# Kernel optimization log

Measured on AMD Instinct MI355X. Metric: run time of the kernel, lower is better.

Reference implementation:

```python
import jax, jax.numpy as jnp
import numpy as np

B, T, D, H, DEPTH, FF, NC = 512, 150, 256, 8, 6, 1024, 4
HD = D // H  # head dim = 32


def setup_inputs() -> dict:
    key = jax.random.key(0)
    ks = iter(jax.random.split(key, 64))
    n = lambda shape, s=0.02: jax.random.normal(next(ks), shape, jnp.float32) * s
    return dict(
        token_types=jax.random.randint(next(ks), (B, T), 0, 4, jnp.int32),
        decision_ids=jax.random.randint(next(ks), (B, T), 0, NC, jnp.int32),
        action_vals=jax.random.normal(next(ks), (B, T, 1), jnp.float32),
        dis_vals=jax.random.normal(next(ks), (B, T, 10), jnp.float32),
        v_vals=jax.random.normal(next(ks), (B, T, 3), jnp.float32),
        action_W=n((1, D), 0.5), action_b=n((D,)),
        dis_W=n((10, D), 0.2), dis_b=n((D,)),
        v_W=n((3, D), 0.3), v_b=n((D,)),
        decision_table=n((NC, D)),
        pos_embed=n((1, T + 1, D)), cls_token=n((1, 1, D)),
        qkv_W=n((DEPTH, D, 3 * D), 0.05), qkv_b=jnp.zeros((DEPTH, 3 * D), jnp.float32),
        out_W=n((DEPTH, D, D), 0.05), out_b=jnp.zeros((DEPTH, D), jnp.float32),
        ln1_g=jnp.ones((DEPTH, D), jnp.float32), ln1_b=jnp.zeros((DEPTH, D), jnp.float32),
        ln2_g=jnp.ones((DEPTH, D), jnp.float32), ln2_b=jnp.zeros((DEPTH, D), jnp.float32),
        ffn1_W=n((DEPTH, D, FF), 0.05), ffn1_b=jnp.zeros((DEPTH, FF), jnp.float32),
        ffn2_W=n((DEPTH, FF, D), 0.05), ffn2_b=jnp.zeros((DEPTH, D), jnp.float32),
        dec_ln_g=jnp.ones((D,), jnp.float32), dec_ln_b=jnp.zeros((D,), jnp.float32),
        dec_W=n((D, NC), 0.05), dec_b=jnp.zeros((NC,), jnp.float32),
        act_ln_g=jnp.ones((D,), jnp.float32), act_ln_b=jnp.zeros((D,), jnp.float32),
        act_W=n((D, 1), 0.05), act_b=jnpp if False else jnp.zeros((1,), jnp.float32),
    )


def _ln(x, g, b):
    # PyTorch LayerNorm: eps=1e-5, biased variance
    m = jnp.mean(x, axis=-1, keepdims=True)
    v = jnp.mean(jnp.square(x - m), axis=-1, keepdims=True)
    return (x - m) * jax.lax.rsqrt(v + 1e-5) * g + b


def reference(token_types, decision_ids, action_vals, dis_vals, v_vals,
              action_W, action_b, dis_W, dis_b, v_W, v_b, decision_table,
              pos_embed, cls_token, qkv_W, qkv_b, out_W, out_b,
              ln1_g, ln1_b, ln2_g, ln2_b, ffn1_W, ffn1_b, ffn2_W, ffn2_b,
              dec_ln_g, dec_ln_b, dec_W, dec_b, act_ln_g, act_ln_b, act_W, act_b):
    # --- batched type-dispatched token embedding (replaces the per-token python loop) ---
    a_emb = action_vals @ action_W + action_b                     # [B,T,D] type 'A'
    s_emb = dis_vals @ dis_W + dis_b + v_vals @ v_W + v_b         # [B,T,D] type 'S'
    d_emb = decision_table[decision_ids]                          # [B,T,D] type 'D'
    t = token_types[..., None]
    x = jnp.where(t == 0, a_emb, jnp.where(t == 1, s_emb, jnp.where(t == 2, d_emb, 0.0)))
    # --- prepend CLS, add positional embedding ---
    x = jnp.concatenate([jnp.broadcast_to(cls_token, (x.shape[0], 1, D)), x], axis=1)
    S = x.shape[1]
    x = x + pos_embed[:, :S, :]
    # --- post-norm TransformerEncoder (PyTorch default: ReLU FFN, norm_first=False, eval/no dropout) ---
    scale = 1.0 / np.sqrt(HD).astype(np.float32)
    for i in range(DEPTH):
        qkv = x @ qkv_W[i] + qkv_b[i]                             # [B,S,3D]
        q, k, v = jnp.split(qkv, 3, axis=-1)
        q = q.reshape(-1, S, H, HD)
        k = k.reshape(-1, S, H, HD)
        v = v.reshape(-1, S, H, HD)
        att = jax.nn.softmax(jnp.einsum('bqhd,bkhd->bhqk', q, k) * scale, axis=-1)
        o = jnp.einsum('bhqk,bkhd->bqhd', att, v).reshape(-1, S, D)
        x = _ln(x + o @ out_W[i] + out_b[i], ln1_g[i], ln1_b[i])
        ff = jax.nn.relu(x @ ffn1_W[i] + ffn1_b[i]) @ ffn2_W[i] + ffn2_b[i]
        x = _ln(x + ff, ln2_g[i], ln2_b[i])
    cls = x[:, 0, :]
    decision_logits = _ln(cls, dec_ln_g, dec_ln_b) @ dec_W + dec_b   # [B,4]
    action_pred = _ln(cls, act_ln_g, act_ln_b) @ act_W + act_b       # [B,1]
    return (decision_logits, action_pred)
```

## Files before the change

kernel.cpp:

```cpp
#include <hip/hip_runtime.h>
#include <hip/hip_bf16.h>

typedef __hip_bfloat16 bf16;
typedef unsigned short u16;
typedef __attribute__((ext_vector_type(8))) short s16x8;
typedef __attribute__((ext_vector_type(4))) float f32x4;

#define B_ 512
#define T_ 150
#define S_ 151
#define D_ 256
#define H_ 8
#define HD_ 32
#define FF_ 1024
#define NC_ 4
#define DEPTH_ 6
#define MTOT 77312
#define MT128 (MTOT / 128)
#define MT64 (MTOT / 64)

#define XOFF 0
#define C1OFF (MTOT * D_)
#define C2OFF (C1OFF + MTOT * FF_)
#define WSELEMS (C2OFF + MTOT * D_)

#define QKVT_OFF 0
#define OUTT_OFF (QKVT_OFF + DEPTH_ * D_ * 768)
#define FFN1T_OFF (OUTT_OFF + DEPTH_ * D_ * D_)
#define FFN2T_OFF (FFN1T_OFF + DEPTH_ * D_ * FF_)
#define WTELEMS (FFN2T_OFF + DEPTH_ * FF_ * D_)

__device__ __align__(16) u16 g_ws[WSELEMS];
__device__ __align__(16) u16 g_wt[WTELEMS];
__device__ int g_f32flag;

__device__ __forceinline__ float ldf(const void* p, size_t i, int f) {
  return f ? ((const float*)p)[i] : __bfloat162float(((const bf16*)p)[i]);
}
__device__ __forceinline__ float b2f(u16 u) {
  union { unsigned int i; float f; } v; v.i = ((unsigned int)u) << 16; return v.f;
}
__device__ __forceinline__ u16 f2b(float x) {
  bf16 h = __float2bfloat16(x);
  return *reinterpret_cast<u16*>(&h);
}

typedef __attribute__((address_space(3))) void lds_void;
typedef const __attribute__((address_space(1))) void glob_void;
__device__ __forceinline__ void gload_lds16(const u16* g, u16* l) {
  __builtin_amdgcn_global_load_lds((glob_void*)g, (lds_void*)l, 16, 0, 0);
}

#define PROBE_N 38656
__global__ __launch_bounds__(256) void probe_kernel(const void* pe)
{
  const u16* w = (const u16*)pe;
  int susp = 0, zeroEven = 0;
  for (int k = threadIdx.x; k < PROBE_N; k += 256) {
    u16 u = w[k];
    int ex = (u >> 7) & 0xFF;
    if (ex >= 141) susp++;
    if ((k & 1) == 0 && (u & 0x7FFF) == 0) zeroEven++;
  }
  __shared__ int s_susp, s_zero;
  if (threadIdx.x == 0) { s_susp = 0; s_zero = 0; }
  __syncthreads();
  atomicAdd(&s_susp, susp);
  atomicAdd(&s_zero, zeroEven);
  __syncthreads();
  if (threadIdx.x == 0)
    g_f32flag = (s_susp > 0 || s_zero >= ((PROBE_N / 2) * 9) / 10) ? 1 : 0;
}

__global__ __launch_bounds__(256) void wtrans_kernel(const void* src, int dstOff,
                                                     int K, int N, int total)
{
  const int f = g_f32flag;
  int idx = blockIdx.x * 256 + threadIdx.x;
  if (idx >= total) return;
  int kn = K * N;
  int l = idx / kn;
  int r = idx - l * kn;
  int k = r / N;
  int n = r - k * N;
  g_wt[dstOff + (size_t)l * kn + (size_t)n * K + k] = f2b(ldf(src, idx, f));
}

__global__ __launch_bounds__(256) void embed_kernel(
    const int* __restrict__ tt, const int* __restrict__ dids,
    const void* av, const void* dv, const void* vv,
    const void* aW, const void* ab, const void* dW, const void* db,
    const void* vW, const void* vb, const void* table, const void* pos,
    const void* cls)
{
  const int f = g_f32flag;
  u16* x = g_ws + XOFF;
  int row = blockIdx.x;
  int d = threadIdx.x;
  int b = row / S_;
  int s = row - b * S_;
  float val;
  if (s == 0) {
    val = ldf(cls, d, f);
  } else {
    int t = s - 1;
    int idx = b * T_ + t;
    int ty = tt[idx];
    if (ty == 0) {
      val = ldf(av, idx, f) * ldf(aW, d, f) + ldf(ab, d, f);
    } else if (ty == 1) {
      float acc = ldf(db, d, f) + ldf(vb, d, f);
#pragma unroll
      for (int i = 0; i < 10; i++) acc += ldf(dv, (size_t)idx * 10 + i, f) * ldf(dW, i * D_ + d, f);
#pragma unroll
      for (int i = 0; i < 3; i++) acc += ldf(vv, (size_t)idx * 3 + i, f) * ldf(vW, i * D_ + d, f);
      val = acc;
    } else if (ty == 2) {
      int did = dids[idx] & (NC_ - 1);
      val = ldf(table, (size_t)did * D_ + d, f);
    } else {
      val = 0.f;
    }
  }
  val += ldf(pos, s * D_ + d, f);
  x[(size_t)row * D_ + d] = f2b(val);
}

__global__ __launch_bounds__(256, 3) void gemm_mfma(
    int aOff, int wtOff, const void* bias, size_t bOff,
    int cOff, int N, int K, int relu, int NB, int tiledC)
{
  const int f = g_f32flag;
  const u16* A = g_ws + aOff;
  const u16* Bt = g_wt + wtOff;
  u16* C = g_ws + cOff;
  __shared__ __align__(16) u16 sm[16384];
  const int tid = threadIdx.x;

  int gblk = blockIdx.x;
  int bm, bn;
  {
    const int full = (MT128 / 8) * 8;
    if (gblk < NB * full) {
      int per = NB * 8;
      int grp = gblk / per, rem = gblk % per;
      bm = grp * 8 + (rem & 7);
      bn = rem >> 3;
    } else {
      int id = gblk - NB * full;
      bm = full + id / NB;
      bn = id % NB;
    }
  }

  const int lane = tid & 63, wid = tid >> 6;
  const int wm = (wid >> 1) * 64, wn = (wid & 1) * 64;
  const int frow = lane & 15, quad = lane >> 4;

  const int rg = lane >> 3;
  const int ck = ((lane & 7) ^ rg) * 8;
  const u16* Ag[4]; const u16* Bg[4];
  u16 *Asl[4], *Bsl[4];
#pragma unroll
  for (int p = 0; p < 4; p++) {
    int grp = wid * 4 + p;
    int row = grp * 8 + rg;
    Ag[p] = A + (size_t)(bm * 128 + row) * K + ck;
    Bg[p] = Bt + (size_t)(bn * 128 + row) * K + ck;
    Asl[p] = &sm[grp * 512];
    Bsl[p] = &sm[8192 + grp * 512];
  }

  f32x4 acc[4][4] = {};

  for (int kt = 0; kt < K; kt += 64) {
    if (kt) __syncthreads();
#pragma unroll
    for (int p = 0; p < 4; p++) {
      gload_lds16(Ag[p] + kt, Asl[p]);
      gload_lds16(Bg[p] + kt, Bsl[p]);
    }
    __syncthreads();
#pragma unroll
    for (int s = 0; s < 2; s++) {
      s16x8 af[4], bfr[4];
      const int cfr = ((s * 4 + quad) ^ (frow & 7)) * 8;
#pragma unroll
      for (int t = 0; t < 4; t++) {
        af[t]  = *(const s16x8*)&sm[(wm + t * 16 + frow) * 64 + cfr];
        bfr[t] = *(const s16x8*)&sm[8192 + (wn + t * 16 + frow) * 64 + cfr];
      }
#pragma unroll
      for (int mt = 0; mt < 4; mt++)
#pragma unroll
        for (int nt = 0; nt < 4; nt++)
          acc[mt][nt] = __builtin_amdgcn_mfma_f32_16x16x32_bf16(af[mt], bfr[nt], acc[mt][nt], 0, 0, 0);
    }
  }

  float bv[4];
#pragma unroll
  for (int nt = 0; nt < 4; nt++)
    bv[nt] = ldf(bias, bOff + (size_t)(bn * 128 + wn + nt * 16 + frow), f);
  __syncthreads();
#pragma unroll
  for (int p = 0; p < 2; p++) {
    if ((wid >> 1) == p) {
#pragma unroll
      for (int mt = 0; mt < 4; mt++)
#pragma unroll
        for (int nt = 0; nt < 4; nt++)
#pragma unroll
          for (int r = 0; r < 4; r++) {
            int rl = (wm & 63) + mt * 16 + quad * 4 + r;
            float v = acc[mt][nt][r] + bv[nt];
            if (relu) v = fmaxf(v, 0.f);
            sm[rl * 136 + wn + nt * 16 + frow] = f2b(v);
          }
    }
    __syncthreads();
    {
      int rl = tid >> 2;
      int cq = (tid & 3) * 32;
      if (!tiledC) {
        size_t gb = (size_t)(bm * 128 + p * 64 + rl) * N + bn * 128 + cq;
#pragma unroll
        for (int j = 0; j < 4; j++)
          *(s16x8*)(C + gb + j * 8) = *(const s16x8*)&sm[rl * 136 + cq + j * 8];
      } else {
        const size_t tmBase = (size_t)(bm * 2 + p) * (N >> 6);
#pragma unroll
        for (int j = 0; j < 4; j++) {
          int col = bn * 128 + cq + j * 8;
          size_t addr = ((tmBase + (col >> 6)) << 12) + (rl << 6) + (col & 63);
          *(s16x8*)(C + addr) = *(const s16x8*)&sm[rl * 136 + cq + j * 8];
        }
      }
    }
    __syncthreads();
  }
}

#define LNHALF 20480

__global__ __launch_bounds__(256, 2) void gemm_ln(
    int aOff, int wtOff, const void* bias, size_t bOff,
    const void* lng, const void* lnb, size_t lnOff, int K)
{
  const int f = g_f32flag;
  const u16* A = g_ws + aOff;
  const u16* Bt = g_wt + wtOff;
  __shared__ __align__(16) u16 sm[2 * LNHALF];
  const int tid = threadIdx.x;
  const int bm = blockIdx.x;
  const int lane = tid & 63, wid = tid >> 6;
  const int wn = wid * 64;
  const int frow = lane & 15, quad = lane >> 4;
  const int rg = lane >> 3;
  const int ck = ((lane & 7) ^ rg) * 8;

  const u16* Ag[2]; u16* Asl[2];
  const u16* Bg[8]; u16* Bsl[8];
#pragma unroll
  for (int p = 0; p < 2; p++) {
    int grp = wid * 2 + p;
    Ag[p] = A + ((size_t)bm * (K >> 6) << 12) + ((grp * 8 + rg) << 6) + ck;
    Asl[p] = &sm[grp * 512];
  }
#pragma unroll
  for (int p = 0; p < 8; p++) {
    int grp = wid * 8 + p;
    Bg[p] = Bt + (size_t)(grp * 8 + rg) * K + ck;
    Bsl[p] = &sm[4096 + grp * 512];
  }

  f32x4 acc[4][4] = {};
  const int nsteps = K >> 6;

#pragma unroll
  for (int p = 0; p < 2; p++) gload_lds16(Ag[p], Asl[p]);
#pragma unroll
  for (int p = 0; p < 8; p++) gload_lds16(Bg[p], Bsl[p]);
  __syncthreads();

  for (int t = 0; t < nsteps; t++) {
    const int cur = (t & 1) * LNHALF;
    if (t + 1 < nsteps) {
      const int nxt = ((t + 1) & 1) * LNHALF;
      const int ktA = (t + 1) << 12;
      const int ktB = (t + 1) << 6;
#pragma unroll
      for (int p = 0; p < 2; p++) gload_lds16(Ag[p] + ktA, Asl[p] + nxt);
#pragma unroll
      for (int p = 0; p < 8; p++) gload_lds16(Bg[p] + ktB, Bsl[p] + nxt);
    }
#pragma unroll
    for (int s = 0; s < 2; s++) {
      s16x8 af[4], bfr[4];
      const int cfr = ((s * 4 + quad) ^ (frow & 7)) * 8;
#pragma unroll
      for (int ti = 0; ti < 4; ti++) {
        af[ti]  = *(const s16x8*)&sm[cur + (ti * 16 + frow) * 64 + cfr];
        bfr[ti] = *(const s16x8*)&sm[cur + 4096 + (wn + ti * 16 + frow) * 64 + cfr];
      }
#pragma unroll
      for (int mt = 0; mt < 4; mt++)
#pragma unroll
        for (int nt = 0; nt < 4; nt++)
          acc[mt][nt] = __builtin_amdgcn_mfma_f32_16x16x32_bf16(af[mt], bfr[nt], acc[mt][nt], 0, 0, 0);
    }
    __syncthreads();
  }

  const int rl = tid >> 2;
  const int cq = (tid & 3) * 64;
  const size_t rowg = (size_t)bm * 64 + rl;
  s16x8 xr[8];
#pragma unroll
  for (int j = 0; j < 8; j++)
    xr[j] = *(const s16x8*)(g_ws + XOFF + rowg * 256 + cq + j * 8);

  float bv[4];
#pragma unroll
  for (int nt = 0; nt < 4; nt++)
    bv[nt] = ldf(bias, bOff + (size_t)(wn + nt * 16 + frow), f);
#pragma unroll
  for (int mt = 0; mt < 4; mt++)
#pragma unroll
    for (int nt = 0; nt < 4; nt++)
#pragma unroll
      for (int r = 0; r < 4; r++) {
        int row = mt * 16 + quad * 4 + r;
        int col = wn + nt * 16 + frow;
        sm[row * 264 + col] = f2b(acc[mt][nt][r] + bv[nt]);
      }
  __syncthreads();
  {
    float s1 = 0.f, s2 = 0.f;
#pragma unroll
    for (int j = 0; j < 8; j++) {
      s16x8 yv = *(const s16x8*)&sm[rl * 264 + cq + j * 8];
#pragma unroll
      for (int e = 0; e < 8; e++) {
        float v = b2f((u16)yv[e]) + b2f((u16)xr[j][e]);
        s1 += v; s2 += v * v;
      }
    }
    s1 += __shfl_xor(s1, 1, 64); s2 += __shfl_xor(s2, 1, 64);
    s1 += __shfl_xor(s1, 2, 64); s2 += __shfl_xor(s2, 2, 64);
    float mean = s1 * (1.f / 256.f);
    float var = s2 * (1.f / 256.f) - mean * mean;
    float rs = rsqrtf(var + 1e-5f);
#pragma unroll
    for (int j = 0; j < 8; j++) {
      s16x8 yv = *(const s16x8*)&sm[rl * 264 + cq + j * 8];
      s16x8 ov;
#pragma unroll
      for (int e = 0; e < 8; e++) {
        float v = b2f((u16)yv[e]) + b2f((u16)xr[j][e]);
        int col = cq + j * 8 + e;
        ov[e] = (short)f2b((v - mean) * rs * ldf(lng, lnOff + col, f) + ldf(lnb, lnOff + col, f));
      }
      *(s16x8*)(g_ws + XOFF + rowg * 256 + cq + j * 8) = ov;
    }
  }
}

#define SP 160
#define KLD 32
#define VLD 170
#define PLDS 42

__global__ __launch_bounds__(320) void attn_kernel()
{
  const u16* qkv = g_ws + C1OFF;
  u16* o = g_ws + C2OFF;
  __shared__ __align__(16) u16 Ks[SP * KLD];
  __shared__ __align__(16) u16 Vt[HD_ * VLD];
  __shared__ __align__(16) u16 Ps[5][16 * PLDS];
  int bh = blockIdx.x;
  int b = bh >> 3, h = bh & 7;
  int tid = threadIdx.x;
  int lane = tid & 63, wid = tid >> 6;
  const u16* base = qkv + (size_t)b * S_ * 768;

  {
    const int jrow = lane >> 2;
    const int dsw = (((lane & 3) ^ ((lane >> 3) & 3)) * 8);
#pragma unroll
    for (int p = 0; p < 2; p++) {
      int g = wid * 2 + p;
      int j = g * 16 + jrow;
      gload_lds16(base + (size_t)j * 768 + 256 + h * 32 + dsw, &Ks[g * 512]);
    }
  }
  for (int g = tid; g < SP * 4; g += 320) {
    int j = g >> 2, d0 = (g & 3) * 8;
    s16x8 vv = {0, 0, 0, 0, 0, 0, 0, 0};
    if (j < S_) vv = *(const s16x8*)(base + (size_t)j * 768 + 512 + h * 32 + d0);
#pragma unroll
    for (int i = 0; i < 8; i++) Vt[(d0 + i) * VLD + j] = (u16)vv[i];
  }
  __syncthreads();

  const int frow = lane & 15;
  const int quad = lane >> 4;
  const int fk = quad * 8;
  const float scale = 0.17677669529663687f;
  u16* Pw = &Ps[wid][0];

  for (int round = 0; round < 2; round++) {
    int mt = round * 5 + wid;
    int qrow = mt * 16 + frow;
    s16x8 aq = {0, 0, 0, 0, 0, 0, 0, 0};
    if (qrow < S_) aq = *(const s16x8*)(base + (size_t)qrow * 768 + h * 32 + fk);
    f32x4 sacc[10];
#pragma unroll
    for (int nt = 0; nt < 10; nt++) {
      s16x8 bk = *(const s16x8*)&Ks[(nt * 16 + frow) * KLD
                                    + ((quad ^ ((frow >> 1) & 3)) * 8)];
      f32x4 z = {0.f, 0.f, 0.f, 0.f};
      sacc[nt] = __builtin_amdgcn_mfma_f32_16x16x32_bf16(aq, bk, z, 0, 0, 0);
    }
#pragma unroll
    for (int nt = 0; nt < 10; nt++) {
      int colg = nt * 16 + frow;
      float msk = (colg < S_) ? 1.f : 0.f;
#pragma unroll
      for (int r = 0; r < 4; r++)
        sacc[nt][r] = msk ? sacc[nt][r] * scale : -1e30f;
    }
    float inv[4];
#pragma unroll
    for (int r = 0; r < 4; r++) {
      float mx = -1e30f;
#pragma unroll
      for (int nt = 0; nt < 10; nt++) mx = fmaxf(mx, sacc[nt][r]);
#pragma unroll
      for (int m = 1; m < 16; m <<= 1) mx = fmaxf(mx, __shfl_xor(mx, m, 64));
      float sm2 = 0.f;
#pragma unroll
      for (int nt = 0; nt < 10; nt++) {
        float p = __expf(sacc[nt][r] - mx);
        sacc[nt][r] = p;
        sm2 += p;
      }
#pragma unroll
      for (int m = 1; m < 16; m <<= 1) sm2 += __shfl_xor(sm2, m, 64);
      inv[r] = 1.f / sm2;
    }
    f32x4 oacc[2] = {};
#pragma unroll
    for (int ks = 0; ks < 5; ks++) {
#pragma unroll
      for (int h2 = 0; h2 < 2; h2++) {
        int nt = ks * 2 + h2;
#pragma unroll
        for (int r = 0; r < 4; r++)
          Pw[(quad * 4 + r) * PLDS + h2 * 16 + frow] = f2b(sacc[nt][r]);
      }
      s16x8 ap = *(const s16x8*)&Pw[frow * PLDS + fk];
#pragma unroll
      for (int nt2 = 0; nt2 < 2; nt2++) {
        s16x8 bv = *(const s16x8*)&Vt[(nt2 * 16 + frow) * VLD + ks * 32 + fk];
        oacc[nt2] = __builtin_amdgcn_mfma_f32_16x16x32_bf16(ap, bv, oacc[nt2], 0, 0, 0);
      }
    }
#pragma unroll
    for (int nt2 = 0; nt2 < 2; nt2++)
#pragma unroll
      for (int r = 0; r < 4; r++) {
        int rowg = mt * 16 + quad * 4 + r;
        if (rowg < S_) {
          int gr = b * S_ + rowg;
          int gc = h * 32 + nt2 * 16 + frow;
          o[(((size_t)(gr >> 6) * (D_ >> 6) + (gc >> 6)) << 12)
            + ((gr & 63) << 6) + (gc & 63)] = f2b(oacc[nt2][r] * inv[r]);
        }
      }
  }
}

__global__ __launch_bounds__(256) void head_kernel(
    const void* dg, const void* dbt, const void* dW, const void* dbias,
    const void* ag, const void* abt, const void* aW, const void* abias,
    void* out)
{
  const int f = g_f32flag;
  const u16* x = g_ws + XOFF;
  int bg = blockIdx.x;
  int tid = threadIdx.x;
  float c = b2f(x[(size_t)bg * S_ * D_ + tid]);
  float s1 = c, s2 = c * c;
#pragma unroll
  for (int off = 32; off > 0; off >>= 1) {
    s1 += __shfl_down(s1, off, 64);
    s2 += __shfl_down(s2, off, 64);
  }
  __shared__ float ws1[4], ws2[4], stats[2];
  __shared__ float lnD[256], lnA[256];
  int wid = tid >> 6, lane = tid & 63;
  if (lane == 0) { ws1[wid] = s1; ws2[wid] = s2; }
  __syncthreads();
  if (tid == 0) {
    float t1 = ws1[0] + ws1[1] + ws1[2] + ws1[3];
    float t2 = ws2[0] + ws2[1] + ws2[2] + ws2[3];
    float mean = t1 * (1.f / 256.f);
    float var = t2 * (1.f / 256.f) - mean * mean;
    stats[0] = mean;
    stats[1] = rsqrtf(var + 1e-5f);
  }
  __syncthreads();
  float n = (c - stats[0]) * stats[1];
  lnD[tid] = n * ldf(dg, tid, f) + ldf(dbt, tid, f);
  lnA[tid] = n * ldf(ag, tid, f) + ldf(abt, tid, f);
  __syncthreads();
  if (tid < NC_) {
    float acc = ldf(dbias, tid, f);
    for (int k = 0; k < D_; k++) acc += lnD[k] * ldf(dW, k * NC_ + tid, f);
    if (f) ((float*)out)[bg * NC_ + tid] = acc;
    else   ((bf16*)out)[bg * NC_ + tid] = __float2bfloat16(acc);
  } else if (tid == 8) {
    float acc = ldf(abias, 0, f);
    for (int k = 0; k < D_; k++) acc += lnA[k] * ldf(aW, k, f);
    if (f) ((float*)out)[B_ * NC_ + bg] = acc;
    else   ((bf16*)out)[B_ * NC_ + bg] = __float2bfloat16(acc);
  }
}

extern "C" void kernel_launch(void* const* d_in, const int* in_sizes, int n_in,
                              void* d_out, int out_size, void* d_ws, size_t ws_size,
                              hipStream_t stream)
{
  (void)in_sizes; (void)out_size; (void)d_ws; (void)ws_size;
  if (n_in < 34) return;
  const int* token_types  = (const int*)d_in[0];
  const int* decision_ids = (const int*)d_in[1];

  probe_kernel<<<1, 256, 0, stream>>>(d_in[12]);

  wtrans_kernel<<<(DEPTH_ * D_ * 768 + 255) / 256, 256, 0, stream>>>(
      d_in[14], QKVT_OFF, D_, 768, DEPTH_ * D_ * 768);
  wtrans_kernel<<<(DEPTH_ * D_ * D_ + 255) / 256, 256, 0, stream>>>(
      d_in[16], OUTT_OFF, D_, D_, DEPTH_ * D_ * D_);
  wtrans_kernel<<<(DEPTH_ * D_ * FF_ + 255) / 256, 256, 0, stream>>>(
      d_in[22], FFN1T_OFF, D_, FF_, DEPTH_ * D_ * FF_);
  wtrans_kernel<<<(DEPTH_ * FF_ * D_ + 255) / 256, 256, 0, stream>>>(
      d_in[24], FFN2T_OFF, FF_, D_, DEPTH_ * FF_ * D_);

  embed_kernel<<<MTOT, 256, 0, stream>>>(token_types, decision_ids,
      d_in[2], d_in[3], d_in[4], d_in[5], d_in[6], d_in[7], d_in[8],
      d_in[9], d_in[10], d_in[11], d_in[12], d_in[13]);

  for (int i = 0; i < DEPTH_; i++) {
    gemm_mfma<<<6 * MT128, 256, 0, stream>>>(XOFF,
        QKVT_OFF + i * D_ * 768, d_in[15], (size_t)i * 768, C1OFF, 768, D_, 0, 6, 0);
    attn_kernel<<<B_ * H_, 320, 0, stream>>>();
    gemm_ln<<<MT64, 256, 0, stream>>>(C2OFF,
        OUTT_OFF + i * D_ * D_, d_in[17], (size_t)i * D_,
        d_in[18], d_in[19], (size_t)i * D_, D_);
    gemm_mfma<<<8 * MT128, 256, 0, stream>>>(XOFF,
        FFN1T_OFF + i * D_ * FF_, d_in[23], (size_t)i * FF_, C1OFF, FF_, D_, 1, 8, 1);
    gemm_ln<<<MT64, 256, 0, stream>>>(C1OFF,
        FFN2T_OFF + i * FF_ * D_, d_in[25], (size_t)i * D_,
        d_in[20], d_in[21], (size_t)i * D_, FF_);
  }
  head_kernel<<<B_, 256, 0, stream>>>(d_in[26], d_in[27], d_in[28], d_in[29],
      d_in[30], d_in[31], d_in[32], d_in[33], d_out);
}
```

Before: 2.480 ms.

## Fuse FFN1, ReLU, FFN2 and LayerNorm into one kernel

```diff
diff --git a/kernel.cpp b/kernel.cpp
--- a/kernel.cpp
+++ b/kernel.cpp
@@ -366,6 +366,162 @@
   }
 }
 
+#define HST 72
+
+__global__ __launch_bounds__(512, 2) void ffn_fused(
+    int w1Off, const void* b1, size_t b1Off,
+    int w2Off, const void* b2, size_t b2Off,
+    const void* lng, const void* lnb, size_t lnOff)
+{
+  const int f = g_f32flag;
+  const u16* W1t = g_wt + w1Off;
+  const u16* W2t = g_wt + w2Off;
+  __shared__ __align__(16) u16 sm[74752];
+  u16* xs  = sm;
+  u16* W1s = sm + 32768;
+  u16* W2s = sm + 49152;
+  u16* hs  = sm + 65536;
+  const int tid = threadIdx.x;
+  const int bm = blockIdx.x;
+  const int lane = tid & 63, wid = tid >> 6;
+  const int frow = lane & 15, quad = lane >> 4;
+  const int rg = lane >> 3;
+  const int ck = ((lane & 7) ^ rg) * 8;
+  const int wrow = (wid >> 2) * 64;
+  const int wcg = wid & 3;
+
+#pragma unroll
+  for (int kt = 0; kt < 4; kt++)
+#pragma unroll
+    for (int p = 0; p < 2; p++) {
+      int grp = wid * 2 + p;
+      gload_lds16(g_ws + XOFF + (size_t)(bm * 128 + grp * 8 + rg) * 256 + kt * 64 + ck,
+                  &xs[kt * 8192 + grp * 512]);
+    }
+#pragma unroll
+  for (int kt = 0; kt < 4; kt++)
+    gload_lds16(W1t + (size_t)(wid * 8 + rg) * 256 + kt * 64 + ck,
+                &W1s[kt * 4096 + wid * 512]);
+#pragma unroll
+  for (int p = 0; p < 4; p++) {
+    int grp = wid * 4 + p;
+    gload_lds16(W2t + (size_t)(grp * 8 + rg) * 1024 + ck, &W2s[grp * 512]);
+  }
+
+  f32x4 acc[4][4] = {};
+
+  for (int c = 0; c < 16; c++) {
+    __syncthreads();
+    f32x4 a1[4] = {};
+#pragma unroll
+    for (int kt = 0; kt < 4; kt++)
+#pragma unroll
+      for (int s = 0; s < 2; s++) {
+        const int cfr = ((s * 4 + quad) ^ (frow & 7)) * 8;
+        s16x8 bf1 = *(const s16x8*)&W1s[kt * 4096 + (wcg * 16 + frow) * 64 + cfr];
+#pragma unroll
+        for (int mt = 0; mt < 4; mt++) {
+          s16x8 af = *(const s16x8*)&xs[kt * 8192 + (wrow + mt * 16 + frow) * 64 + cfr];
+          a1[mt] = __builtin_amdgcn_mfma_f32_16x16x32_bf16(af, bf1, a1[mt], 0, 0, 0);
+        }
+      }
+    {
+      float b1v = ldf(b1, b1Off + c * 64 + wcg * 16 + frow, f);
+#pragma unroll
+      for (int mt = 0; mt < 4; mt++)
+#pragma unroll
+        for (int r = 0; r < 4; r++)
+          hs[(wrow + mt * 16 + quad * 4 + r) * HST + wcg * 16 + frow] =
+              f2b(fmaxf(a1[mt][r] + b1v, 0.f));
+    }
+    __syncthreads();
+    if (c + 1 < 16) {
+#pragma unroll
+      for (int kt = 0; kt < 4; kt++)
+        gload_lds16(W1t + (size_t)((c + 1) * 64 + wid * 8 + rg) * 256 + kt * 64 + ck,
+                    &W1s[kt * 4096 + wid * 512]);
+    }
+#pragma unroll
+    for (int s2 = 0; s2 < 2; s2++) {
+      const int cfr = ((s2 * 4 + quad) ^ (frow & 7)) * 8;
+      s16x8 ap[4], bf2[4];
+#pragma unroll
+      for (int ti = 0; ti < 4; ti++)
+        ap[ti] = *(const s16x8*)&hs[(wrow + ti * 16 + frow) * HST + s2 * 32 + quad * 8];
+#pragma unroll
+      for (int nt = 0; nt < 4; nt++)
+        bf2[nt] = *(const s16x8*)&W2s[(wcg * 64 + nt * 16 + frow) * 64 + cfr];
+#pragma unroll
+      for (int mt = 0; mt < 4; mt++)
+#pragma unroll
+        for (int nt = 0; nt < 4; nt++)
+          acc[mt][nt] = __builtin_amdgcn_mfma_f32_16x16x32_bf16(ap[mt], bf2[nt], acc[mt][nt], 0, 0, 0);
+    }
+    __syncthreads();
+    if (c + 1 < 16) {
+#pragma unroll
+      for (int p = 0; p < 4; p++) {
+        int grp = wid * 4 + p;
+        gload_lds16(W2t + (size_t)(grp * 8 + rg) * 1024 + (c + 1) * 64 + ck,
+                    &W2s[grp * 512]);
+      }
+    }
+  }
+
+  const int rl = tid >> 2;
+  const int cq = (tid & 3) * 64;
+  const size_t rowg = (size_t)bm * 128 + rl;
+  s16x8 xr[8];
+#pragma unroll
+  for (int j = 0; j < 8; j++)
+    xr[j] = *(const s16x8*)(g_ws + XOFF + rowg * 256 + cq + j * 8);
+
+  float bv[4];
+#pragma unroll
+  for (int nt = 0; nt < 4; nt++)
+    bv[nt] = ldf(b2, b2Off + (size_t)(wcg * 64 + nt * 16 + frow), f);
+#pragma unroll
+  for (int mt = 0; mt < 4; mt++)
+#pragma unroll
+    for (int nt = 0; nt < 4; nt++)
+#pragma unroll
+      for (int r = 0; r < 4; r++) {
+        int row = wrow + mt * 16 + quad * 4 + r;
+        int col = wcg * 64 + nt * 16 + frow;
+        sm[row * 264 + col] = f2b(acc[mt][nt][r] + bv[nt]);
+      }
+  __syncthreads();
+  {
+    float s1 = 0.f, s2 = 0.f;
+#pragma unroll
+    for (int j = 0; j < 8; j++) {
+      s16x8 yv = *(const s16x8*)&sm[rl * 264 + cq + j * 8];
+#pragma unroll
+      for (int e = 0; e < 8; e++) {
+        float v = b2f((u16)yv[e]) + b2f((u16)xr[j][e]);
+        s1 += v; s2 += v * v;
+      }
+    }
+    s1 += __shfl_xor(s1, 1, 64); s2 += __shfl_xor(s2, 1, 64);
+    s1 += __shfl_xor(s1, 2, 64); s2 += __shfl_xor(s2, 2, 64);
+    float mean = s1 * (1.f / 256.f);
+    float var = s2 * (1.f / 256.f) - mean * mean;
+    float rs = rsqrtf(var + 1e-5f);
+#pragma unroll
+    for (int j = 0; j < 8; j++) {
+      s16x8 yv = *(const s16x8*)&sm[rl * 264 + cq + j * 8];
+      s16x8 ov;
+#pragma unroll
+      for (int e = 0; e < 8; e++) {
+        float v = b2f((u16)yv[e]) + b2f((u16)xr[j][e]);
+        int col = cq + j * 8 + e;
+        ov[e] = (short)f2b((v - mean) * rs * ldf(lng, lnOff + col, f) + ldf(lnb, lnOff + col, f));
+      }
+      *(s16x8*)(g_ws + XOFF + rowg * 256 + cq + j * 8) = ov;
+    }
+  }
+}
+
 #define SP 160
 #define KLD 32
 #define VLD 170
@@ -559,11 +715,10 @@
     gemm_ln<<<MT64, 256, 0, stream>>>(C2OFF,
         OUTT_OFF + i * D_ * D_, d_in[17], (size_t)i * D_,
         d_in[18], d_in[19], (size_t)i * D_, D_);
-    gemm_mfma<<<8 * MT128, 256, 0, stream>>>(XOFF,
-        FFN1T_OFF + i * D_ * FF_, d_in[23], (size_t)i * FF_, C1OFF, FF_, D_, 1, 8, 1);
-    gemm_ln<<<MT64, 256, 0, stream>>>(C1OFF,
+    ffn_fused<<<MT128, 512, 0, stream>>>(
+        FFN1T_OFF + i * D_ * FF_, d_in[23], (size_t)i * FF_,
         FFN2T_OFF + i * FF_ * D_, d_in[25], (size_t)i * D_,
-        d_in[20], d_in[21], (size_t)i * D_, FF_);
+        d_in[20], d_in[21], (size_t)i * D_);
   }
   head_kernel<<<B_, 256, 0, stream>>>(d_in[26], d_in[27], d_in[28], d_in[29],
       d_in[30], d_in[31], d_in[32], d_in[33], d_out);
```

Result: no change. 2.503 ms (+1.0%).
